# Performance work log

Measured on AMD Instinct MI355X. Metric: run time of the kernel, lower is better.

## Reference

```python
import jax, jax.numpy as jnp
import numpy as np

B, N, D, H = 16, 1024, 768, 12
HD = D // H
SCALE = HD ** -0.5


def setup_inputs() -> dict:
    key = jax.random.key(0)
    ks = jax.random.split(key, 7)
    s = D ** -0.5
    return {
        "x": jax.random.normal(ks[0], (B, N, D), dtype=jnp.float32),
        "Wq": jax.random.normal(ks[1], (D, D), dtype=jnp.float32) * s,
        "bq": jax.random.normal(ks[2], (D,), dtype=jnp.float32) * 0.01,
        "Wk": jax.random.normal(ks[3], (D, D), dtype=jnp.float32) * s,
        "bk": jax.random.normal(ks[4], (D,), dtype=jnp.float32) * 0.01,
        "Wv": jax.random.normal(ks[5], (D, D), dtype=jnp.float32) * s,
        "bv": jax.random.normal(ks[6], (D,), dtype=jnp.float32) * 0.01,
    }


def _split_heads(t):
    # [B, N, D] -> [B, H, N, HD]
    return t.reshape(B, N, H, HD).transpose(0, 2, 1, 3)


def reference(x, Wq, bq, Wk, bk, Wv, bv):
    q = _split_heads(x @ Wq + bq)
    k = _split_heads(x @ Wk + bk)
    v = _split_heads(x @ Wv + bv)
    # [B, H, N, N] attention scores, fp32 softmax (matches eager path)
    scores = jnp.einsum("bhqd,bhkd->bhqk", q, k) * SCALE
    attn = jax.nn.softmax(scores.astype(jnp.float32), axis=-1).astype(q.dtype)
    # dropout p=0 in eval mode -> identity
    ctx = jnp.einsum("bhqk,bhkd->bhqd", attn, v)  # [B, H, N, HD]
    ctx = ctx.transpose(0, 2, 1, 3).reshape(B, N, D)
    return ctx
```

## Files before the change

kernel.cpp:

```cpp
#include <hip/hip_runtime.h>

#define B_ 16
#define N_ 1024
#define D_ 768
#define H_ 12
#define HD_ 64
#define QSCALE 0.18033688011112042f

typedef __attribute__((ext_vector_type(8))) __bf16 bf16x8;
typedef __attribute__((ext_vector_type(4))) float f32x4;
typedef unsigned short u16;
typedef unsigned int u32;

__device__ inline u16 f2bf(float f) {
    u32 u = __builtin_bit_cast(u32, f);
    u += 0x7fffu + ((u >> 16) & 1u);
    return (u16)(u >> 16);
}

__device__ inline float fexp2(float x) {
#if __has_builtin(__builtin_amdgcn_exp2f)
    return __builtin_amdgcn_exp2f(x);
#else
    return exp2f(x);
#endif
}

__device__ inline u32 cvt_pk_bf16(float a, float b) {
    u32 r;
    asm("v_cvt_pk_bf16_f32 %0, %1, %2" : "=v"(r) : "v"(a), "v"(b));
    return r;
}

__device__ inline void gl_lds16(const u16* gp, u16* lp_) {
    __builtin_amdgcn_global_load_lds(
        (const __attribute__((address_space(1))) u32*)(gp),
        (__attribute__((address_space(3))) u32*)(lp_), 16, 0, 0);
}

__global__ __launch_bounds__(256) void prep_kernel(
    const float* __restrict__ x, u16* __restrict__ xbf,
    const float* __restrict__ Wq, const float* __restrict__ Wk,
    const float* __restrict__ Wv, u16* __restrict__ wtall) {
    const int bid = blockIdx.x, tid = threadIdx.x;
    if (bid < 6144) {
        int i = bid * 256 + tid;
        const float4* p = (const float4*)x;
        float4 a = p[2 * i], b = p[2 * i + 1];
        union { u16 us[8]; int4 v; } u;
        u.us[0] = f2bf(a.x); u.us[1] = f2bf(a.y); u.us[2] = f2bf(a.z); u.us[3] = f2bf(a.w);
        u.us[4] = f2bf(b.x); u.us[5] = f2bf(b.y); u.us[6] = f2bf(b.z); u.us[7] = f2bf(b.w);
        ((int4*)xbf)[i] = u.v;
    } else {
        __shared__ u16 t[32][33];
        int wb = bid - 6144;
        int z = wb / 576, rem = wb % 576;
        int bx = rem % 24, by = rem / 24;
        const float* W = z == 0 ? Wq : (z == 1 ? Wk : Wv);
        u16* Wt = wtall + (size_t)z * D_ * D_;
        int n0 = bx * 32, k0 = by * 32;
        int tx = tid & 31, ty = tid >> 5;
#pragma unroll
        for (int i = 0; i < 4; i++) {
            int k = k0 + ty + i * 8;
            t[ty + i * 8][tx] = f2bf(W[k * D_ + n0 + tx]);
        }
        __syncthreads();
#pragma unroll
        for (int i = 0; i < 4; i++) {
            int n = n0 + ty + i * 8;
            Wt[n * D_ + k0 + tx] = t[tx][ty + i * 8];
        }
    }
}

__global__ __launch_bounds__(256) void qkv2_kernel(
    const u16* __restrict__ xbf, const u16* __restrict__ wtall,
    const float* __restrict__ bq, const float* __restrict__ bk, const float* __restrict__ bv,
    u16* __restrict__ qbf, u16* __restrict__ kbf, u16* __restrict__ vtbf) {
    __shared__ u16 lsA[4 * 4096];
    __shared__ u16 lsB[4 * 4096];

    const int mt = blockIdx.x, nt = blockIdx.y;
    const int tid = threadIdx.x, w = tid >> 6, lane = tid & 63;
    const int g = lane >> 4, c = lane & 15;
    const int wr = w >> 1, wc = w & 1;
    const int m0 = mt * 128, n0 = nt * 128;

    const int row0 = tid >> 2, cp0 = tid & 3;
    const u16* ba0 = xbf + (size_t)(m0 + row0) * D_ + cp0 * 8;
    const u16* ba1 = xbf + (size_t)(m0 + row0 + 64) * D_ + cp0 * 8;
    const u16* bb0 = wtall + (size_t)(n0 + row0) * D_ + cp0 * 8;
    const u16* bb1 = wtall + (size_t)(n0 + row0 + 64) * D_ + cp0 * 8;

#define STAGEP(slot, p) do {                                   \
        gl_lds16(ba0 + (p) * 32, &lsA[(slot) * 4096 + w * 512]);        \
        gl_lds16(ba1 + (p) * 32, &lsA[(slot) * 4096 + 2048 + w * 512]); \
        gl_lds16(bb0 + (p) * 32, &lsB[(slot) * 4096 + w * 512]);        \
        gl_lds16(bb1 + (p) * 32, &lsB[(slot) * 4096 + 2048 + w * 512]); \
    } while (0)

    f32x4 acc[4][4];
#pragma unroll
    for (int i = 0; i < 4; i++)
#pragma unroll
        for (int j = 0; j < 4; j++) acc[i][j] = (f32x4){0.f, 0.f, 0.f, 0.f};

#define COMPUTE(s) do {                                                         \
        bf16x8 af[4], bfr[4];                                                   \
        _Pragma("unroll")                                                       \
        for (int f = 0; f < 4; f++)                                             \
            af[f] = *(const bf16x8*)&lsA[(s) * 4096 + (wr * 64 + f * 16 + c) * 32 + g * 8]; \
        _Pragma("unroll")                                                       \
        for (int f = 0; f < 4; f++)                                             \
            bfr[f] = *(const bf16x8*)&lsB[(s) * 4096 + (wc * 64 + f * 16 + c) * 32 + g * 8]; \
        _Pragma("unroll")                                                       \
        for (int fr = 0; fr < 4; fr++)                                          \
            _Pragma("unroll")                                                   \
            for (int fc = 0; fc < 4; fc++)                                      \
                acc[fr][fc] = __builtin_amdgcn_mfma_f32_16x16x32_bf16(          \
                    af[fr], bfr[fc], acc[fr][fc], 0, 0, 0);                     \
    } while (0)

    STAGEP(0, 0);
    STAGEP(1, 1);
    for (int p = 0; p < 22; ++p) {
        STAGEP((p + 2) & 3, p + 2);
        asm volatile("s_waitcnt vmcnt(8)" ::: "memory");
        __builtin_amdgcn_s_barrier();
        __builtin_amdgcn_sched_barrier(0);
        COMPUTE(p & 3);
    }
    asm volatile("s_waitcnt vmcnt(4)" ::: "memory");
    __builtin_amdgcn_s_barrier();
    __builtin_amdgcn_sched_barrier(0);
    COMPUTE(2);
    asm volatile("s_waitcnt vmcnt(0)" ::: "memory");
    __builtin_amdgcn_s_barrier();
    __builtin_amdgcn_sched_barrier(0);
    COMPUTE(3);
#undef STAGEP
#undef COMPUTE

    const int mode = nt / 6;
    const int ncol0 = (nt % 6) * 128;
    const float* bias = mode == 0 ? bq : (mode == 1 ? bk : bv);
    float bb[4];
#pragma unroll
    for (int fc = 0; fc < 4; fc++) bb[fc] = bias[ncol0 + wc * 64 + fc * 16 + c];

    if (mode < 2) {
        u16* outp = mode == 0 ? qbf : kbf;
        const float osc = mode == 0 ? QSCALE : 1.0f;
#pragma unroll
        for (int fc = 0; fc < 4; fc++) {
            int col = ncol0 + wc * 64 + fc * 16 + c;
            int head = col >> 6, hd = col & 63;
#pragma unroll
            for (int fr = 0; fr < 4; fr++)
#pragma unroll
                for (int rr = 0; rr < 4; rr++) {
                    int m = m0 + wr * 64 + fr * 16 + g * 4 + rr;
                    int b = m >> 10, nn = m & 1023;
                    outp[(((size_t)b * H_ + head) * N_ + nn) * HD_ + hd] =
                        f2bf((acc[fr][fc][rr] + bb[fc]) * osc);
                }
        }
    } else {
#pragma unroll
        for (int fc = 0; fc < 4; fc++) {
            int col = ncol0 + wc * 64 + fc * 16 + c;
            int head = col >> 6, hd = col & 63;
#pragma unroll
            for (int fr = 0; fr < 4; fr++) {
                int m = m0 + wr * 64 + fr * 16 + g * 4;
                int b = m >> 10, nn = m & 1023;
                union { u16 us[4]; int2 v; } u;
#pragma unroll
                for (int rr = 0; rr < 4; rr++) u.us[rr] = f2bf(acc[fr][fc][rr] + bb[fc]);
                *(int2*)&vtbf[(((size_t)b * H_ + head) * HD_ + hd) * N_ + nn] = u.v;
            }
        }
    }
}

__global__ __launch_bounds__(256) void attn_kernel(
    const u16* __restrict__ qbf, const u16* __restrict__ kbf,
    const u16* __restrict__ vtbf, float* __restrict__ out) {
    __shared__ u16 lk[2][64][72];
    __shared__ u16 lv[2][64][72];

    const int bh = blockIdx.x;
    const int qt = blockIdx.y;
    const int b = bh / H_, h = bh % H_;
    const int tid = threadIdx.x;
    const int w = tid >> 6, lane = tid & 63, g = lane >> 4, c = lane & 15;
    const int q0 = qt * 128;

    bf16x8 aq[2][2];
#pragma unroll
    for (int ss = 0; ss < 2; ss++) {
        const u16* qr = qbf + ((size_t)bh * N_ + q0 + w * 32 + ss * 16 + c) * HD_;
        aq[ss][0] = *(const bf16x8*)&qr[g * 8];
        aq[ss][1] = *(const bf16x8*)&qr[32 + g * 8];
    }

    const u16* kbase = kbf + (size_t)bh * N_ * HD_;
    const u16* vbase = vtbf + (size_t)bh * HD_ * N_;
    const int r0 = tid >> 3, c80 = (tid & 7) * 8;
    const int r1 = r0 + 32;

    int4 kreg0, kreg1, vreg0, vreg1;
#define LOADT(KV) do { \
        kreg0 = *(const int4*)(kbase + (size_t)((KV) + r0) * HD_ + c80); \
        kreg1 = *(const int4*)(kbase + (size_t)((KV) + r1) * HD_ + c80); \
        vreg0 = *(const int4*)(vbase + (size_t)r0 * N_ + (KV) + c80); \
        vreg1 = *(const int4*)(vbase + (size_t)r1 * N_ + (KV) + c80); \
    } while (0)
#define WRITET(bi) do { \
        *(int4*)&lk[bi][r0][c80] = kreg0; \
        *(int4*)&lk[bi][r1][c80] = kreg1; \
        *(int4*)&lv[bi][r0][c80] = vreg0; \
        *(int4*)&lv[bi][r1][c80] = vreg1; \
    } while (0)

    const f32x4 zf = (f32x4){0.f, 0.f, 0.f, 0.f};
    f32x4 o[2][4];
#pragma unroll
    for (int ss = 0; ss < 2; ss++)
#pragma unroll
        for (int i = 0; i < 4; i++) o[ss][i] = zf;
    float lr[2] = {0.f, 0.f};

    LOADT(0);
    WRITET(0);
    __syncthreads();
    int cur = 0;

    for (int kv0 = 0; kv0 < N_; kv0 += 64) {
        const bool more = (kv0 + 64) < N_;
        if (more) LOADT(kv0 + 64);

        f32x4 sc[2][4];
#pragma unroll
        for (int nf = 0; nf < 4; nf++) {
            bf16x8 ak0 = *(const bf16x8*)&lk[cur][nf * 16 + c][g * 8];
            bf16x8 ak1 = *(const bf16x8*)&lk[cur][nf * 16 + c][32 + g * 8];
            __builtin_amdgcn_s_setprio(1);
#pragma unroll
            for (int ss = 0; ss < 2; ss++) {
                sc[ss][nf] = __builtin_amdgcn_mfma_f32_16x16x32_bf16(ak0, aq[ss][0], zf, 0, 0, 0);
                sc[ss][nf] = __builtin_amdgcn_mfma_f32_16x16x32_bf16(ak1, aq[ss][1], sc[ss][nf], 0, 0, 0);
            }
            __builtin_amdgcn_s_setprio(0);
        }

        u32 pkk[2][4][2];
#pragma unroll
        for (int ss = 0; ss < 2; ss++) {
            f32x4 rsv = zf;
#pragma unroll
            for (int nf = 0; nf < 4; nf++) {
#pragma unroll
                for (int r = 0; r < 4; r++) sc[ss][nf][r] = fexp2(sc[ss][nf][r]);
                rsv += sc[ss][nf];
                pkk[ss][nf][0] = cvt_pk_bf16(sc[ss][nf][0], sc[ss][nf][1]);
                pkk[ss][nf][1] = cvt_pk_bf16(sc[ss][nf][2], sc[ss][nf][3]);
            }
            lr[ss] += (rsv[0] + rsv[1]) + (rsv[2] + rsv[3]);
        }

        bf16x8 pa[2][2];
#pragma unroll
        for (int ss = 0; ss < 2; ss++) {
            union { u32 ui[4]; bf16x8 v; } u0, u1;
            u0.ui[0] = pkk[ss][0][0]; u0.ui[1] = pkk[ss][0][1];
            u0.ui[2] = pkk[ss][1][0]; u0.ui[3] = pkk[ss][1][1];
            u1.ui[0] = pkk[ss][2][0]; u1.ui[1] = pkk[ss][2][1];
            u1.ui[2] = pkk[ss][3][0]; u1.ui[3] = pkk[ss][3][1];
            pa[ss][0] = u0.v; pa[ss][1] = u1.v;
        }

#pragma unroll
        for (int nf = 0; nf < 4; nf++) {
            union { int2 d[2]; bf16x8 v; } b0, b1;
            b0.d[0] = *(const int2*)&lv[cur][nf * 16 + c][4 * g];
            b0.d[1] = *(const int2*)&lv[cur][nf * 16 + c][16 + 4 * g];
            b1.d[0] = *(const int2*)&lv[cur][nf * 16 + c][32 + 4 * g];
            b1.d[1] = *(const int2*)&lv[cur][nf * 16 + c][48 + 4 * g];
            __builtin_amdgcn_s_setprio(1);
#pragma unroll
            for (int ss = 0; ss < 2; ss++) {
                o[ss][nf] = __builtin_amdgcn_mfma_f32_16x16x32_bf16(pa[ss][0], b0.v, o[ss][nf], 0, 0, 0);
                o[ss][nf] = __builtin_amdgcn_mfma_f32_16x16x32_bf16(pa[ss][1], b1.v, o[ss][nf], 0, 0, 0);
            }
            __builtin_amdgcn_s_setprio(0);
        }

        if (more) WRITET(cur ^ 1);
        __syncthreads();
        cur ^= 1;
    }
#undef LOADT
#undef WRITET

#pragma unroll
    for (int ss = 0; ss < 2; ss++) {
        float lf = lr[ss];
        lf += __shfl_xor(lf, 16);
        lf += __shfl_xor(lf, 32);
        float lq[4];
#pragma unroll
        for (int r = 0; r < 4; r++) lq[r] = __shfl(lf, g * 4 + r);
#pragma unroll
        for (int r = 0; r < 4; r++) {
            float inv = 1.f / lq[r];
            int n = q0 + w * 32 + ss * 16 + g * 4 + r;
#pragma unroll
            for (int nf = 0; nf < 4; nf++)
                out[((size_t)(b * N_ + n)) * D_ + h * HD_ + nf * 16 + c] = o[ss][nf][r] * inv;
        }
    }
}

extern "C" void kernel_launch(void* const* d_in, const int* in_sizes, int n_in,
                              void* d_out, int out_size, void* d_ws, size_t ws_size,
                              hipStream_t stream) {
    const float* x  = (const float*)d_in[0];
    const float* Wq = (const float*)d_in[1];
    const float* bq = (const float*)d_in[2];
    const float* Wk = (const float*)d_in[3];
    const float* bk = (const float*)d_in[4];
    const float* Wv = (const float*)d_in[5];
    const float* bv = (const float*)d_in[6];
    float* out = (float*)d_out;

    char* ws = (char*)d_ws;
    u16* xbf   = (u16*)ws;
    u16* wtall = (u16*)(ws + 25165824);
    u16* qbf   = (u16*)(ws + 28704768);
    u16* kbf   = (u16*)(ws + 53870592);
    u16* vtbf  = (u16*)(ws + 79036416);

    prep_kernel<<<7872, 256, 0, stream>>>(x, xbf, Wq, Wk, Wv, wtall);
    dim3 gg(128, 18);
    qkv2_kernel<<<gg, 256, 0, stream>>>(xbf, wtall, bq, bk, bv, qbf, kbf, vtbf);
    dim3 ga(192, 8);
    attn_kernel<<<ga, 256, 0, stream>>>(qbf, kbf, vtbf, out);
}
```

Baseline: 175.5 us.

## Enlarge QKV GEMM tile to 256x192 with 8 waves and swizzled LDS

The QKV projection GEMM moves from 128x128 tiles with 4 waves to 256x192 tiles with 8 waves (512 threads). Each wave now computes 128x48, giving more reuse per LDS load and cutting the grid from 2304 to 768 blocks. An XOR swizzle on the 16-byte chunk index is applied consistently on the global-to-LDS staging and on the fragment reads, to reduce LDS bank conflicts. In exchange, LDS use doubles to 128 KB per block, which limits occupancy, and there are fewer blocks to spread across the CUs.

```diff
diff --git a/kernel.cpp b/kernel.cpp
--- a/kernel.cpp
+++ b/kernel.cpp
@@ -74,50 +74,53 @@
     }
 }
 
-__global__ __launch_bounds__(256) void qkv2_kernel(
+__global__ __launch_bounds__(512, 2) void qkv2_kernel(
     const u16* __restrict__ xbf, const u16* __restrict__ wtall,
     const float* __restrict__ bq, const float* __restrict__ bk, const float* __restrict__ bv,
     u16* __restrict__ qbf, u16* __restrict__ kbf, u16* __restrict__ vtbf) {
-    __shared__ u16 lsA[4 * 4096];
-    __shared__ u16 lsB[4 * 4096];
+    __shared__ u16 lsA[4 * 8192];
+    __shared__ u16 lsB[4 * 8192];
 
     const int mt = blockIdx.x, nt = blockIdx.y;
     const int tid = threadIdx.x, w = tid >> 6, lane = tid & 63;
     const int g = lane >> 4, c = lane & 15;
-    const int wr = w >> 1, wc = w & 1;
-    const int m0 = mt * 128, n0 = nt * 128;
-
-    const int row0 = tid >> 2, cp0 = tid & 3;
-    const u16* ba0 = xbf + (size_t)(m0 + row0) * D_ + cp0 * 8;
-    const u16* ba1 = xbf + (size_t)(m0 + row0 + 64) * D_ + cp0 * 8;
-    const u16* bb0 = wtall + (size_t)(n0 + row0) * D_ + cp0 * 8;
-    const u16* bb1 = wtall + (size_t)(n0 + row0 + 64) * D_ + cp0 * 8;
-
-#define STAGEP(slot, p) do {                                   \
-        gl_lds16(ba0 + (p) * 32, &lsA[(slot) * 4096 + w * 512]);        \
-        gl_lds16(ba1 + (p) * 32, &lsA[(slot) * 4096 + 2048 + w * 512]); \
-        gl_lds16(bb0 + (p) * 32, &lsB[(slot) * 4096 + w * 512]);        \
-        gl_lds16(bb1 + (p) * 32, &lsB[(slot) * 4096 + 2048 + w * 512]); \
+    const int wm = w >> 2, wn = w & 3;
+    const int m0 = mt * 256, n0 = nt * 192;
+
+    const int srow = w * 16 + (lane >> 2);
+    const int gch = (lane & 3) ^ ((lane >> 3) & 3);
+    const u16* sa0 = xbf + (size_t)(m0 + srow) * D_ + gch * 8;
+    const u16* sa1 = xbf + (size_t)(m0 + 128 + srow) * D_ + gch * 8;
+    const u16* sb0 = wtall + (size_t)(n0 + srow) * D_ + gch * 8;
+    const u16* sb1 = wtall + (size_t)(n0 + 128 + srow) * D_ + gch * 8;
+
+#define STAGEP(slot, p) do {                                          \
+        gl_lds16(sa0 + (p) * 32, &lsA[(slot) * 8192 + w * 512]);        \
+        gl_lds16(sa1 + (p) * 32, &lsA[(slot) * 8192 + 4096 + w * 512]); \
+        gl_lds16(sb0 + (p) * 32, &lsB[(slot) * 8192 + w * 512]);        \
+        gl_lds16(sb1 + (p) * 32, &lsB[(slot) * 8192 + 4096 + w * 512]); \
     } while (0)
 
-    f32x4 acc[4][4];
-#pragma unroll
-    for (int i = 0; i < 4; i++)
-#pragma unroll
-        for (int j = 0; j < 4; j++) acc[i][j] = (f32x4){0.f, 0.f, 0.f, 0.f};
+    f32x4 acc[8][3];
+#pragma unroll
+    for (int i = 0; i < 8; i++)
+#pragma unroll
+        for (int j = 0; j < 3; j++) acc[i][j] = (f32x4){0.f, 0.f, 0.f, 0.f};
+
+    const int gp8 = (g ^ ((c >> 1) & 3)) * 8;
 
 #define COMPUTE(s) do {                                                         \
-        bf16x8 af[4], bfr[4];                                                   \
+        bf16x8 af[8], bfr[3];                                                   \
         _Pragma("unroll")                                                       \
-        for (int f = 0; f < 4; f++)                                             \
-            af[f] = *(const bf16x8*)&lsA[(s) * 4096 + (wr * 64 + f * 16 + c) * 32 + g * 8]; \
+        for (int fr = 0; fr < 8; fr++)                                          \
+            af[fr] = *(const bf16x8*)&lsA[(s) * 8192 + (wm * 128 + fr * 16 + c) * 32 + gp8]; \
         _Pragma("unroll")                                                       \
-        for (int f = 0; f < 4; f++)                                             \
-            bfr[f] = *(const bf16x8*)&lsB[(s) * 4096 + (wc * 64 + f * 16 + c) * 32 + g * 8]; \
+        for (int fc = 0; fc < 3; fc++)                                          \
+            bfr[fc] = *(const bf16x8*)&lsB[(s) * 8192 + (wn * 48 + fc * 16 + c) * 32 + gp8]; \
         _Pragma("unroll")                                                       \
-        for (int fr = 0; fr < 4; fr++)                                          \
+        for (int fr = 0; fr < 8; fr++)                                          \
             _Pragma("unroll")                                                   \
-            for (int fc = 0; fc < 4; fc++)                                      \
+            for (int fc = 0; fc < 3; fc++)                                      \
                 acc[fr][fc] = __builtin_amdgcn_mfma_f32_16x16x32_bf16(          \
                     af[fr], bfr[fc], acc[fr][fc], 0, 0, 0);                     \
     } while (0)
@@ -142,25 +145,25 @@
 #undef STAGEP
 #undef COMPUTE
 
-    const int mode = nt / 6;
-    const int ncol0 = (nt % 6) * 128;
+    const int mode = nt >> 2;
+    const int msub = nt & 3;
     const float* bias = mode == 0 ? bq : (mode == 1 ? bk : bv);
-    float bb[4];
-#pragma unroll
-    for (int fc = 0; fc < 4; fc++) bb[fc] = bias[ncol0 + wc * 64 + fc * 16 + c];
+    float bb[3];
+#pragma unroll
+    for (int fc = 0; fc < 3; fc++) bb[fc] = bias[msub * 192 + wn * 48 + fc * 16 + c];
 
     if (mode < 2) {
         u16* outp = mode == 0 ? qbf : kbf;
         const float osc = mode == 0 ? QSCALE : 1.0f;
 #pragma unroll
-        for (int fc = 0; fc < 4; fc++) {
-            int col = ncol0 + wc * 64 + fc * 16 + c;
+        for (int fc = 0; fc < 3; fc++) {
+            int col = msub * 192 + wn * 48 + fc * 16 + c;
             int head = col >> 6, hd = col & 63;
 #pragma unroll
-            for (int fr = 0; fr < 4; fr++)
+            for (int fr = 0; fr < 8; fr++)
 #pragma unroll
                 for (int rr = 0; rr < 4; rr++) {
-                    int m = m0 + wr * 64 + fr * 16 + g * 4 + rr;
+                    int m = m0 + wm * 128 + fr * 16 + g * 4 + rr;
                     int b = m >> 10, nn = m & 1023;
                     outp[(((size_t)b * H_ + head) * N_ + nn) * HD_ + hd] =
                         f2bf((acc[fr][fc][rr] + bb[fc]) * osc);
@@ -168,12 +171,12 @@
         }
     } else {
 #pragma unroll
-        for (int fc = 0; fc < 4; fc++) {
-            int col = ncol0 + wc * 64 + fc * 16 + c;
+        for (int fc = 0; fc < 3; fc++) {
+            int col = msub * 192 + wn * 48 + fc * 16 + c;
             int head = col >> 6, hd = col & 63;
 #pragma unroll
-            for (int fr = 0; fr < 4; fr++) {
-                int m = m0 + wr * 64 + fr * 16 + g * 4;
+            for (int fr = 0; fr < 8; fr++) {
+                int m = m0 + wm * 128 + fr * 16 + g * 4;
                 int b = m >> 10, nn = m & 1023;
                 union { u16 us[4]; int2 v; } u;
 #pragma unroll
@@ -343,8 +346,8 @@
     u16* vtbf  = (u16*)(ws + 79036416);
 
     prep_kernel<<<7872, 256, 0, stream>>>(x, xbf, Wq, Wk, Wv, wtall);
-    dim3 gg(128, 18);
-    qkv2_kernel<<<gg, 256, 0, stream>>>(xbf, wtall, bq, bk, bv, qbf, kbf, vtbf);
+    dim3 gg(64, 12);
+    qkv2_kernel<<<gg, 512, 0, stream>>>(xbf, wtall, bq, bk, bv, qbf, kbf, vtbf);
     dim3 ga(192, 8);
     attn_kernel<<<ga, 256, 0, stream>>>(qbf, kbf, vtbf, out);
 }
```

After: 167.4 us, median of 2. -4.6%, faster.
